# Kernel optimization log

Hardware: AMD Instinct MI355X
Metric: run time of the kernel (lower is better)

Reference implementation:

```python
import jax, jax.numpy as jnp
import numpy as np

SPATIAL_SHAPES = [(160, 160), (80, 80), (40, 40)]
D_MODEL = 256
N_HEADS = 8
N_LEVELS = 3
N_POINTS = 4
B = 1
SEQ = sum(h * w for h, w in SPATIAL_SHAPES)  # 33600


def setup_inputs() -> dict:
    key = jax.random.key(0)
    ks = jax.random.split(key, 10)
    f = jax.random.normal
    return {
        "hidden_states": f(ks[0], (B, SEQ, D_MODEL), jnp.float32),
        "encoder_hidden_states": f(ks[1], (B, SEQ, D_MODEL), jnp.float32),
        "position_embeddings": f(ks[2], (B, SEQ, D_MODEL), jnp.float32),
        "reference_points": jax.random.uniform(ks[3], (B, SEQ, N_LEVELS, 2), jnp.float32),
        "Wv": f(ks[4], (D_MODEL, D_MODEL), jnp.float32) * 0.02,
        "bv": jnp.zeros((D_MODEL,), jnp.float32),
        "Ws": f(ks[5], (N_HEADS * N_LEVELS * N_POINTS * 2, D_MODEL), jnp.float32) * 0.02,
        "bs": f(ks[6], (N_HEADS * N_LEVELS * N_POINTS * 2,), jnp.float32) * 2.0,
        "Wa": f(ks[7], (N_HEADS * N_LEVELS * N_POINTS, D_MODEL), jnp.float32) * 0.02,
        "ba": jnp.zeros((N_HEADS * N_LEVELS * N_POINTS,), jnp.float32),
        "Wo": f(ks[8], (D_MODEL, D_MODEL), jnp.float32) * 0.02,
        "bo": jnp.zeros((D_MODEL,), jnp.float32),
    }


def grid_sample_bilinear(img, grid):
    """torch.nn.functional.grid_sample, mode='bilinear', padding_mode='zeros', align_corners=False.
    img: [N, C, Hi, Wi]; grid: [N, Hg, Wg, 2] with (x, y) in [-1, 1]. Returns [N, C, Hg, Wg]."""
    N, C, Hi, Wi = img.shape
    x = (grid[..., 0] + 1.0) * (Wi * 0.5) - 0.5  # unnormalized pixel coords
    y = (grid[..., 1] + 1.0) * (Hi * 0.5) - 0.5
    x0f = jnp.floor(x)
    y0f = jnp.floor(y)
    x0 = x0f.astype(jnp.int32)
    y0 = y0f.astype(jnp.int32)
    wx1 = x - x0f
    wy1 = y - y0f
    imgc = jnp.transpose(img, (0, 2, 3, 1))  # [N, Hi, Wi, C]
    n_idx = jnp.arange(N)[:, None, None]

    def tap(xi, yi, w):
        valid = (xi >= 0) & (xi < Wi) & (yi >= 0) & (yi < Hi)
        xc = jnp.clip(xi, 0, Wi - 1)
        yc = jnp.clip(yi, 0, Hi - 1)
        v = imgc[n_idx, yc, xc]  # [N, Hg, Wg, C]
        return v * (w * valid.astype(img.dtype))[..., None]

    out = (tap(x0, y0, (1.0 - wx1) * (1.0 - wy1))
           + tap(x0 + 1, y0, wx1 * (1.0 - wy1))
           + tap(x0, y0 + 1, (1.0 - wx1) * wy1)
           + tap(x0 + 1, y0 + 1, wx1 * wy1))
    return jnp.transpose(out, (0, 3, 1, 2))  # [N, C, Hg, Wg]


def reference(hidden_states, encoder_hidden_states, position_embeddings, reference_points,
              Wv, bv, Ws, bs, Wa, ba, Wo, bo):
    hd = D_MODEL // N_HEADS
    LP = N_LEVELS * N_POINTS
    Q = SEQ

    hs = hidden_states + position_embeddings  # [B, Q, D]
    value = (encoder_hidden_states @ Wv.T + bv).reshape(B, SEQ, N_HEADS, hd)
    offsets = (hs @ Ws.T + bs).reshape(B * Q, N_HEADS, LP, 2)
    attn = jax.nn.softmax((hs @ Wa.T + ba).reshape(B, Q, N_HEADS, LP), axis=-1)

    # offset normalizer: [w, h] per level, broadcast over points
    norm = jnp.array([[w, h] for (h, w) in SPATIAL_SHAPES], jnp.float32)  # [L, 2]
    norm = jnp.broadcast_to(norm[:, None, :], (N_LEVELS, N_POINTS, 2)).reshape(1, 1, LP, 2)
    rp = reference_points.reshape(-1, N_LEVELS, 1, 2)
    rp = jnp.broadcast_to(rp, (B * Q, N_LEVELS, N_POINTS, 2)).reshape(B * Q, 1, LP, 2)
    loc = rp + offsets / norm                # [BQ, H, LP, 2]
    grids = 2.0 * loc - 1.0

    attn_t = jnp.transpose(attn, (0, 2, 1, 3)).reshape(B * N_HEADS, 1, Q, LP)

    sampled = []
    start = 0
    for lvl, (h, w) in enumerate(SPATIAL_SHAPES):
        v = value[:, start:start + h * w].reshape(B, h * w, N_HEADS * hd)
        v = jnp.transpose(v, (0, 2, 1)).reshape(B * N_HEADS, hd, h, w)
        g = jnp.transpose(grids[:, :, lvl * N_POINTS:(lvl + 1) * N_POINTS], (1, 0, 2, 3))  # [H, BQ, P, 2] (B=1)
        sampled.append(grid_sample_bilinear(v, g))  # [B*H, hd, Q, P]
        start += h * w

    out = (jnp.concatenate(sampled, axis=-1) * attn_t).sum(-1)  # [B*H, hd, Q]
    out = jnp.transpose(out.reshape(B, N_HEADS * hd, Q), (0, 2, 1))  # [B, Q, D]
    output = out @ Wo.T + bo
    return output, attn
```

## Files before the change

### kernel.cpp

```cpp
#include <hip/hip_runtime.h>
#include <math.h>

#define QSEQ 33600

typedef __attribute__((ext_vector_type(8))) short short8;
typedef __attribute__((ext_vector_type(4))) float floatx4;
typedef unsigned short ushort_t;

static __device__ __forceinline__ ushort_t f2bf(float f) {
  unsigned u = __float_as_uint(f);
  return (ushort_t)((u + 0x7FFF + ((u >> 16) & 1)) >> 16);
}

static __device__ __forceinline__ unsigned pk2bf(float lo, float hi) {
  unsigned r;
  asm("v_cvt_pk_bf16_f32 %0, %1, %2" : "=v"(r) : "v"(lo), "v"(hi));
  return r;
}

static __device__ __forceinline__ short8 cvt8(const float4 x0, const float4 x1) {
  union { unsigned u[4]; short8 s; } r;
  r.u[0] = pk2bf(x0.x, x0.y);
  r.u[1] = pk2bf(x0.z, x0.w);
  r.u[2] = pk2bf(x1.x, x1.y);
  r.u[3] = pk2bf(x1.z, x1.w);
  return r.s;
}

static __device__ __forceinline__ float4 add4(float4 a, const float4 b) {
  a.x += b.x; a.y += b.y; a.z += b.z; a.w += b.w;
  return a;
}

template <int ASRC, int MODE>
static __device__ __forceinline__ void gemm_body(
    const int bx, const int by,
    const float* __restrict__ A1, const float* __restrict__ A2,
    const ushort_t* __restrict__ Ab,
    const float* __restrict__ B1, const float* __restrict__ B2, const int bsplit,
    const float* __restrict__ b1, const float* __restrict__ b2,
    void* __restrict__ C1, float* __restrict__ C2, const int N,
    ushort_t* smem) {
  const int tid = threadIdx.x;
  const int m0 = by * 96;
  const int n0 = bx * 128;
  const int wv = tid >> 6, lane = tid & 63;
  const int wm = wv >> 1, wn = wv & 1;
  const int l16 = lane & 15, quad = lane >> 4;
  const int l8 = l16 & 7;

#pragma unroll
  for (int it = 0; it < 16; ++it) {
    const int c = tid + it * 256;
    const int row = c >> 5, kc = c & 31;
    const int grow = n0 + row;
    const float* bsrc;
    int r2;
    if (grow < bsplit) {
      bsrc = B1;
      r2 = grow;
    } else {
      bsrc = B2;
      r2 = grow - bsplit;
      const int rmax = N - bsplit - 1;
      if (r2 > rmax) r2 = rmax;
    }
    const float* src = bsrc + (size_t)r2 * 256 + kc * 8;
    const float4 x0 = *(const float4*)src;
    const float4 x1 = *(const float4*)(src + 4);
    const short8 v = cvt8(x0, x1);
    *(short8*)&smem[(row * 32 + (kc ^ (row & 7))) * 8] = v;
  }
  __syncthreads();

  const float* pA[3];
  const float* pA2[3];
  const ushort_t* pAb[3];
#pragma unroll
  for (int mi = 0; mi < 3; ++mi) {
    const int rr = m0 + wm * 48 + mi * 16 + l16;
    if (ASRC == 0) {
      pAb[mi] = Ab + (size_t)rr * 256 + quad * 8;
    } else {
      pA[mi] = A1 + (size_t)rr * 256 + quad * 8;
      if (ASRC == 2) pA2[mi] = A2 + (size_t)rr * 256 + quad * 8;
    }
  }
  int brow[4];
#pragma unroll
  for (int ni = 0; ni < 4; ++ni) brow[ni] = (wn * 64 + ni * 16 + l16) * 256;

  floatx4 acc[3][4];
#pragma unroll
  for (int i = 0; i < 3; ++i)
#pragma unroll
    for (int j = 0; j < 4; ++j) acc[i][j] = (floatx4)(0.f);

#pragma unroll
  for (int k32 = 0; k32 < 8; ++k32) {
    short8 a[3], b[4];
#pragma unroll
    for (int mi = 0; mi < 3; ++mi) {
      if (ASRC == 0) {
        a[mi] = *(const short8*)(pAb[mi] + k32 * 32);
      } else {
        float4 x0 = *(const float4*)(pA[mi] + k32 * 32);
        float4 x1 = *(const float4*)(pA[mi] + k32 * 32 + 4);
        if (ASRC == 2) {
          x0 = add4(x0, *(const float4*)(pA2[mi] + k32 * 32));
          x1 = add4(x1, *(const float4*)(pA2[mi] + k32 * 32 + 4));
        }
        a[mi] = cvt8(x0, x1);
      }
    }
#pragma unroll
    for (int ni = 0; ni < 4; ++ni) {
      const int slot = ((k32 << 2) | quad) ^ l8;
      b[ni] = *(const short8*)&smem[brow[ni] + slot * 8];
    }
#pragma unroll
    for (int mi = 0; mi < 3; ++mi)
#pragma unroll
      for (int ni = 0; ni < 4; ++ni)
        acc[mi][ni] = __builtin_amdgcn_mfma_f32_16x16x32_bf16(a[mi], b[ni], acc[mi][ni], 0, 0, 0);
  }

  if (MODE == 0) {
    float* C = (float*)C1;
#pragma unroll
    for (int ni = 0; ni < 4; ++ni) {
      const int col = n0 + wn * 64 + ni * 16 + l16;
      const float bia = b1[col];
#pragma unroll
      for (int mi = 0; mi < 3; ++mi) {
        const int rr = m0 + wm * 48 + mi * 16 + quad * 4;
#pragma unroll
        for (int r = 0; r < 4; ++r)
          C[(size_t)(rr + r) * N + col] = acc[mi][ni][r] + bia;
      }
    }
  } else if (MODE == 1) {
    ushort_t* C = (ushort_t*)C1;
#pragma unroll
    for (int ni = 0; ni < 4; ++ni) {
      const int col = n0 + wn * 64 + ni * 16 + l16;
      const float bia = b1[col];
      const int h = col >> 5, ch = col & 31;
#pragma unroll
      for (int mi = 0; mi < 3; ++mi) {
        const int rr = m0 + wm * 48 + mi * 16 + quad * 4;
#pragma unroll
        for (int r = 0; r < 4; ++r)
          C[((size_t)h * QSEQ + rr + r) * 32 + ch] = f2bf(acc[mi][ni][r] + bia);
      }
    }
  } else {
    __syncthreads();
    float* smf = (float*)smem;
#pragma unroll
    for (int ni = 0; ni < 4; ++ni) {
      const int col = n0 + wn * 64 + ni * 16 + l16;
      if (col < 96) {
        const float bia = b1[col];
#pragma unroll
        for (int mi = 0; mi < 3; ++mi) {
          const int lr = wm * 48 + mi * 16 + quad * 4;
#pragma unroll
          for (int r = 0; r < 4; ++r)
            smf[(lr + r) * 96 + col] = acc[mi][ni][r] + bia;
        }
      } else if (col < 288) {
        const float bia = b2[col - 96];
#pragma unroll
        for (int mi = 0; mi < 3; ++mi) {
          const int rr = m0 + wm * 48 + mi * 16 + quad * 4;
#pragma unroll
          for (int r = 0; r < 4; ++r)
            C2[(size_t)(rr + r) * 192 + (col - 96)] = acc[mi][ni][r] + bia;
        }
      }
    }
    __syncthreads();
    if (bx == 0) {
      float* C = (float*)C1;
#pragma unroll
      for (int p = 0; p < 3; ++p) {
        const int task = tid + p * 256;
        const int row = task >> 3, hh = task & 7;
        float v[12];
        float mx = -1e30f;
#pragma unroll
        for (int i = 0; i < 12; ++i) {
          v[i] = smf[row * 96 + hh * 12 + i];
          mx = fmaxf(mx, v[i]);
        }
        float s = 0.f;
#pragma unroll
        for (int i = 0; i < 12; ++i) {
          v[i] = __expf(v[i] - mx);
          s += v[i];
        }
        const float inv = 1.f / s;
        float4 o[3];
#pragma unroll
        for (int i = 0; i < 3; ++i) {
          o[i].x = v[i * 4 + 0] * inv;
          o[i].y = v[i * 4 + 1] * inv;
          o[i].z = v[i * 4 + 2] * inv;
          o[i].w = v[i * 4 + 3] * inv;
        }
        float4* dst = (float4*)&C[(size_t)(m0 + row) * 96 + hh * 12];
        dst[0] = o[0];
        dst[1] = o[1];
        dst[2] = o[2];
      }
    }
  }
}

__global__ __launch_bounds__(256, 2) void pre_gemms(
    const float* __restrict__ ehs, const float* __restrict__ hidden,
    const float* __restrict__ pos,
    const float* __restrict__ Wv, const float* __restrict__ bv,
    const float* __restrict__ Wa, const float* __restrict__ ba,
    const float* __restrict__ Ws, const float* __restrict__ bs,
    ushort_t* __restrict__ value, float* __restrict__ attn,
    float* __restrict__ sp) {
  extern __shared__ ushort_t smem[];
  const int bid = blockIdx.x;
  const int xcd = bid & 7, idx = bid >> 3;
  const int work = (xcd < 6 ? xcd * 219 : 1314 + (xcd - 6) * 218) + idx;
  if (work < 700)
    gemm_body<1, 1>(work & 1, work >> 1, ehs, nullptr, nullptr,
                    Wv, Wv, 1 << 30, bv, nullptr, value, nullptr, 256, smem);
  else {
    const int w2 = work - 700;
    gemm_body<2, 2>(w2 % 3, w2 / 3, hidden, pos, nullptr,
                    Wa, Ws, 96, ba, bs, attn, sp, 288, smem);
  }
}

__global__ __launch_bounds__(256, 2) void out_gemm(
    const ushort_t* __restrict__ samp, const float* __restrict__ Wo,
    const float* __restrict__ bo, float* __restrict__ out) {
  extern __shared__ ushort_t smem[];
  const int bid = blockIdx.x;
  const int xcd = bid & 7, idx = bid >> 3;
  const int work = (xcd < 4 ? xcd * 88 : 352 + (xcd - 4) * 87) + idx;
  gemm_body<0, 0>(work & 1, work >> 1, nullptr, nullptr, samp,
                  Wo, Wo, 1 << 30, bo, nullptr, out, nullptr, 256, smem);
}

__global__ __launch_bounds__(256) void msda_sample_kernel(
    const ushort_t* __restrict__ value,
    const float* __restrict__ sp,
    const float* __restrict__ attn,
    const float* __restrict__ refp,
    ushort_t* __restrict__ outp) {
  __shared__ unsigned wtab[32 * 100];
  const int tid = threadIdx.x;
  const int h = blockIdx.x & 7;
  const int qbase = (blockIdx.x >> 3) * 32;

#pragma unroll
  for (int pass = 0; pass < 2; ++pass) {
    const int it = tid + pass * 256;
    if (it < 384) {
      const int tq = it / 12;
      const int pt = it - tq * 12;
      const int q = qbase + tq;
      const int lvl = pt >> 2;
      const int S = lvl == 0 ? 160 : (lvl == 1 ? 80 : 40);
      const int base = lvl == 0 ? 0 : (lvl == 1 ? 25600 : 32000);

      const float a = attn[q * 96 + h * 12 + pt];
      const float2 off = *(const float2*)&sp[q * 192 + h * 24 + pt * 2];
      const float2 rp = *(const float2*)&refp[q * 6 + lvl * 2];

      const float x = fmaf(rp.x, (float)S, off.x) - 0.5f;
      const float y = fmaf(rp.y, (float)S, off.y) - 0.5f;
      const float xf = floorf(x), yf = floorf(y);
      const int x0 = (int)xf, y0 = (int)yf;
      const float wx1 = x - xf, wy1 = y - yf;

      const float wx0z = (x0 >= 0 && x0 < S) ? 1.f - wx1 : 0.f;
      const float wx1z = (x0 + 1 >= 0 && x0 + 1 < S) ? wx1 : 0.f;
      const float wy0z = (y0 >= 0 && y0 < S) ? 1.f - wy1 : 0.f;
      const float wy1z = (y0 + 1 >= 0 && y0 + 1 < S) ? wy1 : 0.f;

      const int x0c = min(max(x0, 0), S - 1);
      const int x1c = min(max(x0 + 1, 0), S - 1);
      const int y0c = min(max(y0, 0), S - 1);
      const int y1c = min(max(y0 + 1, 0), S - 1);

      const int r0 = base + y0c * S, r1 = base + y1c * S;
      uint4 e0, e1;
      e0.x = __float_as_uint(a * wx0z * wy0z);
      e0.y = (unsigned)(r0 + x0c) << 6;
      e0.z = __float_as_uint(a * wx1z * wy0z);
      e0.w = (unsigned)(r0 + x1c) << 6;
      e1.x = __float_as_uint(a * wx0z * wy1z);
      e1.y = (unsigned)(r1 + x0c) << 6;
      e1.z = __float_as_uint(a * wx1z * wy1z);
      e1.w = (unsigned)(r1 + x1c) << 6;
      unsigned* dst = &wtab[tq * 100 + pt * 8];
      *(uint4*)dst = e0;
      *(uint4*)(dst + 4) = e1;
    }
  }
  __syncthreads();

  const int wv = tid >> 6;
  const int qi = (tid >> 3) & 7;
  const int c = tid & 7;
  const int tq = wv * 8 + qi;
  const int q = qbase + tq;
  const unsigned* wt = &wtab[tq * 100];
  const char* vbase = (const char*)value + ((size_t)h * QSEQ) * 64 + c * 8;

  float f0 = 0.f, f1 = 0.f, f2 = 0.f, f3 = 0.f;
#pragma unroll
  for (int r = 0; r < 48; ++r) {
    const uint2 e = *(const uint2*)&wt[r * 2];
    const float w = __uint_as_float(e.x);
    const uint2 v = *(const uint2*)(vbase + e.y);
    f0 = fmaf(__uint_as_float(v.x << 16), w, f0);
    f1 = fmaf(__uint_as_float(v.x & 0xFFFF0000u), w, f1);
    f2 = fmaf(__uint_as_float(v.y << 16), w, f2);
    f3 = fmaf(__uint_as_float(v.y & 0xFFFF0000u), w, f3);
  }

  ushort_t t[4] = {f2bf(f0), f2bf(f1), f2bf(f2), f2bf(f3)};
  *(uint2*)&outp[(size_t)q * 256 + h * 32 + c * 4] = *(const uint2*)t;
}

extern "C" void kernel_launch(void* const* d_in, const int* in_sizes, int n_in,
                              void* d_out, int out_size, void* d_ws, size_t ws_size,
                              hipStream_t stream) {
  const float* hidden = (const float*)d_in[0];
  const float* ehs    = (const float*)d_in[1];
  const float* pos    = (const float*)d_in[2];
  const float* refp   = (const float*)d_in[3];
  const float* Wv = (const float*)d_in[4];
  const float* bv = (const float*)d_in[5];
  const float* Ws = (const float*)d_in[6];
  const float* bs = (const float*)d_in[7];
  const float* Wa = (const float*)d_in[8];
  const float* ba = (const float*)d_in[9];
  const float* Wo = (const float*)d_in[10];
  const float* bo = (const float*)d_in[11];

  float* out  = (float*)d_out;
  float* attn = out + (size_t)QSEQ * 256;

  char* ws = (char*)d_ws;
  ushort_t* ws_value = (ushort_t*)ws;
  ushort_t* ws_outp  = ws_value + (size_t)QSEQ * 256;
  float* ws_sp = (float*)(ws_outp + (size_t)QSEQ * 256);

  dim3 blk(256);

  pre_gemms<<<dim3(1750), blk, 65536, stream>>>(
      ehs, hidden, pos, Wv, bv, Wa, ba, Ws, bs, ws_value, attn, ws_sp);
  msda_sample_kernel<<<dim3((QSEQ / 32) * 8), blk, 0, stream>>>(
      ws_value, ws_sp, attn, refp, ws_outp);
  out_gemm<<<dim3(700), blk, 65536, stream>>>(ws_outp, Wo, bo, out);
}
```

Measured before the change: 322.2 us.

## Pre-convert GEMM activations to bf16 and preload A fragments into registers

Adds a prep kernel that converts encoder_hidden_states and hidden+pos to bf16 once, staging them in the output buffer before it is overwritten. The GEMMs then read bf16 A operands, and each thread loads all eight k-slices of A into registers up front, separated from the MFMA loop by a sched_barrier. The intent is to halve A-read traffic in the GEMMs and remove the repeated fp32 add and convert work. It costs an extra launch plus a write and re-read of two bf16 arrays, more register pressure, and drops the two-blocks-per-CU launch bound.

```diff
diff --git a/kernel.cpp b/kernel.cpp
--- a/kernel.cpp
+++ b/kernel.cpp
@@ -32,10 +32,21 @@
   return a;
 }
 
-template <int ASRC, int MODE>
+__global__ __launch_bounds__(256) void prep_bf16(
+    const float* __restrict__ ehs, const float* __restrict__ hidden,
+    const float* __restrict__ pos, ushort_t* __restrict__ ehs_b,
+    ushort_t* __restrict__ hs_b) {
+  const size_t c = (size_t)blockIdx.x * 256 + threadIdx.x;
+  const float4* pe = (const float4*)ehs + c * 2;
+  const float4* ph = (const float4*)hidden + c * 2;
+  const float4* pp = (const float4*)pos + c * 2;
+  *(short8*)(ehs_b + c * 8) = cvt8(pe[0], pe[1]);
+  *(short8*)(hs_b + c * 8) = cvt8(add4(ph[0], pp[0]), add4(ph[1], pp[1]));
+}
+
+template <int MODE>
 static __device__ __forceinline__ void gemm_body(
     const int bx, const int by,
-    const float* __restrict__ A1, const float* __restrict__ A2,
     const ushort_t* __restrict__ Ab,
     const float* __restrict__ B1, const float* __restrict__ B2, const int bsplit,
     const float* __restrict__ b1, const float* __restrict__ b2,
@@ -66,26 +77,24 @@
       if (r2 > rmax) r2 = rmax;
     }
     const float* src = bsrc + (size_t)r2 * 256 + kc * 8;
-    const float4 x0 = *(const float4*)src;
-    const float4 x1 = *(const float4*)(src + 4);
-    const short8 v = cvt8(x0, x1);
-    *(short8*)&smem[(row * 32 + (kc ^ (row & 7))) * 8] = v;
+    *(short8*)&smem[(row * 32 + (kc ^ (row & 7))) * 8] =
+        cvt8(*(const float4*)src, *(const float4*)(src + 4));
   }
   __syncthreads();
 
-  const float* pA[3];
-  const float* pA2[3];
   const ushort_t* pAb[3];
 #pragma unroll
-  for (int mi = 0; mi < 3; ++mi) {
-    const int rr = m0 + wm * 48 + mi * 16 + l16;
-    if (ASRC == 0) {
-      pAb[mi] = Ab + (size_t)rr * 256 + quad * 8;
-    } else {
-      pA[mi] = A1 + (size_t)rr * 256 + quad * 8;
-      if (ASRC == 2) pA2[mi] = A2 + (size_t)rr * 256 + quad * 8;
-    }
-  }
+  for (int mi = 0; mi < 3; ++mi)
+    pAb[mi] = Ab + (size_t)(m0 + wm * 48 + mi * 16 + l16) * 256 + quad * 8;
+
+  short8 aReg[8][3];
+#pragma unroll
+  for (int k32 = 0; k32 < 8; ++k32)
+#pragma unroll
+    for (int mi = 0; mi < 3; ++mi)
+      aReg[k32][mi] = *(const short8*)(pAb[mi] + k32 * 32);
+  __builtin_amdgcn_sched_barrier(0);
+
   int brow[4];
 #pragma unroll
   for (int ni = 0; ni < 4; ++ni) brow[ni] = (wn * 64 + ni * 16 + l16) * 256;
@@ -98,31 +107,17 @@
 
 #pragma unroll
   for (int k32 = 0; k32 < 8; ++k32) {
-    short8 a[3], b[4];
-#pragma unroll
-    for (int mi = 0; mi < 3; ++mi) {
-      if (ASRC == 0) {
-        a[mi] = *(const short8*)(pAb[mi] + k32 * 32);
-      } else {
-        float4 x0 = *(const float4*)(pA[mi] + k32 * 32);
-        float4 x1 = *(const float4*)(pA[mi] + k32 * 32 + 4);
-        if (ASRC == 2) {
-          x0 = add4(x0, *(const float4*)(pA2[mi] + k32 * 32));
-          x1 = add4(x1, *(const float4*)(pA2[mi] + k32 * 32 + 4));
-        }
-        a[mi] = cvt8(x0, x1);
-      }
-    }
-#pragma unroll
-    for (int ni = 0; ni < 4; ++ni) {
-      const int slot = ((k32 << 2) | quad) ^ l8;
+    const int slot = ((k32 << 2) | quad) ^ l8;
+    short8 b[4];
+#pragma unroll
+    for (int ni = 0; ni < 4; ++ni)
       b[ni] = *(const short8*)&smem[brow[ni] + slot * 8];
-    }
 #pragma unroll
     for (int mi = 0; mi < 3; ++mi)
 #pragma unroll
       for (int ni = 0; ni < 4; ++ni)
-        acc[mi][ni] = __builtin_amdgcn_mfma_f32_16x16x32_bf16(a[mi], b[ni], acc[mi][ni], 0, 0, 0);
+        acc[mi][ni] = __builtin_amdgcn_mfma_f32_16x16x32_bf16(
+            aReg[k32][mi], b[ni], acc[mi][ni], 0, 0, 0);
   }
 
   if (MODE == 0) {
@@ -218,9 +213,8 @@
   }
 }
 
-__global__ __launch_bounds__(256, 2) void pre_gemms(
-    const float* __restrict__ ehs, const float* __restrict__ hidden,
-    const float* __restrict__ pos,
+__global__ __launch_bounds__(256) void pre_gemms(
+    const ushort_t* __restrict__ ehs_b, const ushort_t* __restrict__ hs_b,
     const float* __restrict__ Wv, const float* __restrict__ bv,
     const float* __restrict__ Wa, const float* __restrict__ ba,
     const float* __restrict__ Ws, const float* __restrict__ bs,
@@ -231,24 +225,24 @@
   const int xcd = bid & 7, idx = bid >> 3;
   const int work = (xcd < 6 ? xcd * 219 : 1314 + (xcd - 6) * 218) + idx;
   if (work < 700)
-    gemm_body<1, 1>(work & 1, work >> 1, ehs, nullptr, nullptr,
-                    Wv, Wv, 1 << 30, bv, nullptr, value, nullptr, 256, smem);
+    gemm_body<1>(work & 1, work >> 1, ehs_b,
+                 Wv, Wv, 1 << 30, bv, nullptr, value, nullptr, 256, smem);
   else {
     const int w2 = work - 700;
-    gemm_body<2, 2>(w2 % 3, w2 / 3, hidden, pos, nullptr,
-                    Wa, Ws, 96, ba, bs, attn, sp, 288, smem);
-  }
-}
-
-__global__ __launch_bounds__(256, 2) void out_gemm(
+    gemm_body<2>(w2 % 3, w2 / 3, hs_b,
+                 Wa, Ws, 96, ba, bs, attn, sp, 288, smem);
+  }
+}
+
+__global__ __launch_bounds__(256) void out_gemm(
     const ushort_t* __restrict__ samp, const float* __restrict__ Wo,
     const float* __restrict__ bo, float* __restrict__ out) {
   extern __shared__ ushort_t smem[];
   const int bid = blockIdx.x;
   const int xcd = bid & 7, idx = bid >> 3;
   const int work = (xcd < 4 ? xcd * 88 : 352 + (xcd - 4) * 87) + idx;
-  gemm_body<0, 0>(work & 1, work >> 1, nullptr, nullptr, samp,
-                  Wo, Wo, 1 << 30, bo, nullptr, out, nullptr, 256, smem);
+  gemm_body<0>(work & 1, work >> 1, samp,
+               Wo, Wo, 1 << 30, bo, nullptr, out, nullptr, 256, smem);
 }
 
 __global__ __launch_bounds__(256) void msda_sample_kernel(
@@ -358,10 +352,14 @@
   ushort_t* ws_outp  = ws_value + (size_t)QSEQ * 256;
   float* ws_sp = (float*)(ws_outp + (size_t)QSEQ * 256);
 
+  ushort_t* ehs_b = (ushort_t*)out;
+  ushort_t* hs_b  = ehs_b + (size_t)QSEQ * 256;
+
   dim3 blk(256);
 
+  prep_bf16<<<dim3(4200), blk, 0, stream>>>(ehs, hidden, pos, ehs_b, hs_b);
   pre_gemms<<<dim3(1750), blk, 65536, stream>>>(
-      ehs, hidden, pos, Wv, bv, Wa, ba, Ws, bs, ws_value, attn, ws_sp);
+      ehs_b, hs_b, Wv, bv, Wa, ba, Ws, bs, ws_value, attn, ws_sp);
   msda_sample_kernel<<<dim3((QSEQ / 32) * 8), blk, 0, stream>>>(
       ws_value, ws_sp, attn, refp, ws_outp);
   out_gemm<<<dim3(700), blk, 65536, stream>>>(ws_outp, Wo, bo, out);
```

After: 274.1 us. 1.18x faster.
